# Performance work log

Hardware: AMD Instinct MI355X
Metric: run time of the kernel (lower is better)

Reference implementation:

```python
import jax, jax.numpy as jnp
import numpy as np

B, C, N, H = 4, 256, 2048, 8
D = C // 4  # q/k projection dim
BN_EPS = 1e-5


def setup_inputs() -> dict:
    key = jax.random.key(0)
    ks = jax.random.split(key, 16)
    s = lambda fan: 1.0 / np.sqrt(fan)
    return {
        "x": jax.random.normal(ks[0], (B, C, N), dtype=jnp.float32),
        # per-head params, stacked on leading head axis
        "w_qk": jax.random.normal(ks[1], (H, D, C), dtype=jnp.float32) * s(C),  # shared q/k conv weight
        "w_v": jax.random.normal(ks[2], (H, C, C), dtype=jnp.float32) * s(C),
        "b_v": jax.random.normal(ks[3], (H, C), dtype=jnp.float32) * 0.01,
        "w_t": jax.random.normal(ks[4], (H, C, C), dtype=jnp.float32) * s(C),
        "b_t": jax.random.normal(ks[5], (H, C), dtype=jnp.float32) * 0.01,
        "bn_g": jnp.ones((H, C), dtype=jnp.float32),
        "bn_b": jnp.zeros((H, C), dtype=jnp.float32),
        "bn_m": jax.random.normal(ks[6], (H, C), dtype=jnp.float32) * 0.1,
        "bn_v": jax.random.uniform(ks[7], (H, C), dtype=jnp.float32, minval=0.5, maxval=1.5),
        # final 1x1 conv + BN (LeakyReLU 0.2)
        "w_lin": jax.random.normal(ks[8], (C, C * H), dtype=jnp.float32) * s(C * H),
        "lbn_g": jnp.ones((C,), dtype=jnp.float32),
        "lbn_b": jnp.zeros((C,), dtype=jnp.float32),
        "lbn_m": jax.random.normal(ks[9], (C,), dtype=jnp.float32) * 0.1,
        "lbn_v": jax.random.uniform(ks[10], (C,), dtype=jnp.float32, minval=0.5, maxval=1.5),
    }


def _oa_head(x, w_qk, w_v, b_v, w_t, b_t, g, b, m, v):
    # x: [B, C, N]; 1x1 Conv1d == channel matmul
    x_q = jnp.einsum("dc,bcn->bnd", w_qk, x)                 # [B, N, D]
    x_k = jnp.einsum("dc,bcn->bdn", w_qk, x)                 # [B, D, N] (shared weight)
    x_v = jnp.einsum("ec,bcn->ben", w_v, x) + b_v[:, None]   # [B, C, N]
    energy = jnp.einsum("bnd,bdm->bnm", x_q, x_k)            # [B, N, N]
    attn = jax.nn.softmax(energy, axis=-1)
    attn = attn / (1e-9 + attn.sum(axis=1, keepdims=True))   # extra L1 renorm over dim=1
    x_r = jnp.einsum("ben,bnm->bem", x_v, attn)              # [B, C, N]
    y = jnp.einsum("ec,bcn->ben", w_t, x - x_r) + b_t[:, None]
    y = (y - m[:, None]) * (g[:, None] / jnp.sqrt(v[:, None] + BN_EPS)) + b[:, None]
    return x + jax.nn.relu(y)


def reference(x, w_qk, w_v, b_v, w_t, b_t, bn_g, bn_b, bn_m, bn_v,
              w_lin, lbn_g, lbn_b, lbn_m, lbn_v):
    # run all H heads via vmap over stacked params -> [B, H, C, N]
    heads = jax.vmap(_oa_head, in_axes=(None, 0, 0, 0, 0, 0, 0, 0, 0, 0), out_axes=1)(
        x, w_qk, w_v, b_v, w_t, b_t, bn_g, bn_b, bn_m, bn_v)
    cat = heads.reshape(x.shape[0], H * C, x.shape[2])       # torch.cat(dim=1) order
    y = jnp.einsum("ck,bkn->bcn", w_lin, cat)                # 1x1 conv, no bias
    y = (y - lbn_m[:, None]) * (lbn_g[:, None] / jnp.sqrt(lbn_v[:, None] + BN_EPS)) + lbn_b[:, None]
    return jnp.where(y >= 0, y, 0.2 * y)                     # LeakyReLU(0.2)
```

## Files before the change

kernel.cpp:

```cpp
#include <hip/hip_runtime.h>
#include <math.h>

#define B_ 4
#define C_ 256
#define N_ 2048
#define H_ 8
#define D_ 64
#define BH_ 32
#define HC_ 2048
#define BN_EPS 1e-5f
#define SCL 1.2011224087864498f

typedef __attribute__((ext_vector_type(8))) short s8v;
typedef __attribute__((ext_vector_type(4))) short s4v;
typedef __attribute__((ext_vector_type(8))) _Float16 h8v;
typedef __attribute__((ext_vector_type(4))) _Float16 h4v;
typedef __attribute__((ext_vector_type(4))) float f32x4;

#define MFMA __builtin_amdgcn_mfma_f32_16x16x32_bf16
#define MFMAH __builtin_amdgcn_mfma_f32_16x16x32_f16

static __device__ __forceinline__ unsigned short f2b(float f) {
  union { float f; unsigned int i; } v; v.f = f;
  unsigned int r = v.i + 0x7FFFu + ((v.i >> 16) & 1u);
  return (unsigned short)(r >> 16);
}
static __device__ __forceinline__ float fexp2(float x) {
  float r;
  asm("v_exp_f32 %0, %1" : "=v"(r) : "v"(x));
  return r;
}
static __device__ __forceinline__ unsigned cvtpk(float lo, float hi) {
  unsigned r;
  asm("v_cvt_pk_bf16_f32 %0, %1, %2" : "=v"(r) : "v"(lo), "v"(hi));
  return r;
}
static __device__ __forceinline__ void gload16(const void* g, void* l) {
  __builtin_amdgcn_global_load_lds(
      (const __attribute__((address_space(1))) unsigned int*)g,
      (__attribute__((address_space(3))) unsigned int*)l, 16, 0, 0);
}

struct GP {
  const float *x, *w_qk, *w_v, *b_v, *w_t, *b_t, *bn_g, *bn_b, *bn_m, *bn_v;
  const float *w_lin, *lbn_g, *lbn_b, *lbn_m, *lbn_v;
  _Float16 *PT, *xT, *wqk16, *wvh;
  short *HOT, *wtb, *wlinb, *Vb, *xmr;
  float *part, *shb, *nrm, *sh, *out;
};

__global__ __launch_bounds__(256) void prep_k(GP p) {
  int u = blockIdx.x * 256 + threadIdx.x;
  if (u < 131072) {
    int i = u * 4;
    float4 v = *(const float4*)(p.w_t + i);
    s4v o = { (short)f2b(v.x), (short)f2b(v.y), (short)f2b(v.z), (short)f2b(v.w) };
    *(s4v*)(p.wtb + i) = o;
  } else if (u < 262144) {
    int i = (u - 131072) * 4;
    float4 v = *(const float4*)(p.w_lin + i);
    s4v o = { (short)f2b(v.x), (short)f2b(v.y), (short)f2b(v.z), (short)f2b(v.w) };
    *(s4v*)(p.wlinb + i) = o;
  } else if (u < 393216) {
    int i = (u - 262144) * 4;
    float4 v = *(const float4*)(p.w_v + i);
    h4v o = { (_Float16)v.x, (_Float16)v.y, (_Float16)v.z, (_Float16)v.w };
    *(h4v*)(p.wvh + i) = o;
  } else {
    int i = (u - 393216) * 4;
    float4 v = *(const float4*)(p.w_qk + i);
    h4v o = { (_Float16)v.x, (_Float16)v.y, (_Float16)v.z, (_Float16)v.w };
    *(h4v*)(p.wqk16 + i) = o;
  }
}

__global__ __launch_bounds__(256) void xcvt_k(const float* __restrict__ x,
                                              _Float16* __restrict__ xT) {
  const int n0 = blockIdx.x * 64, c0 = blockIdx.y * 64, b = blockIdx.z;
  const float* xb = x + (size_t)b * C_ * N_;
  __shared__ float sm[64][65];
  const int t = threadIdx.x;
#pragma unroll
  for (int i = 0; i < 4; ++i) {
    int idx = i * 256 + t;
    int c = idx >> 4, j = (idx & 15) * 4;
    float4 v = *(const float4*)(xb + (size_t)(c0 + c) * N_ + n0 + j);
    sm[j + 0][c] = v.x; sm[j + 1][c] = v.y; sm[j + 2][c] = v.z; sm[j + 3][c] = v.w;
  }
  __syncthreads();
#pragma unroll
  for (int i = 0; i < 2; ++i) {
    int idx = i * 256 + t;
    int n = idx >> 3, cg = (idx & 7) * 8;
    h8v o;
#pragma unroll
    for (int d = 0; d < 8; ++d) o[d] = (_Float16)sm[n][cg + d];
    *(h8v*)(xT + ((size_t)b * N_ + n0 + n) * C_ + c0 + cg) = o;
  }
}

__global__ __launch_bounds__(256, 2) void p_k(GP p) {
  const int t = threadIdx.x, wv = t >> 6, lane = t & 63;
  const int l15 = lane & 15, l4 = lane >> 4;
  const int n0 = blockIdx.x * 128;
  const int bh = blockIdx.y, b = bh / H_, h = bh % H_;
  const _Float16* Ag = p.wqk16 + h * D_ * C_;
  const _Float16* Bg = p.xT + (size_t)b * N_ * C_;
  __shared__ _Float16 As[64 * 64], Bs[128 * 64];
  __shared__ float Tr[128 * 65];
  f32x4 acc[4][2] = {};
  for (int kc = 0; kc < 256; kc += 64) {
    __syncthreads();
#pragma unroll
    for (int i = 0; i < 2; ++i) {
      int idx = i * 256 + t;
      int row = idx >> 3, offl = (idx & 7) * 16;
      gload16((const char*)(Ag + (size_t)row * C_ + kc) + (offl ^ ((row & 7) << 4)),
              (char*)As + idx * 16);
    }
#pragma unroll
    for (int i = 0; i < 4; ++i) {
      int idx = i * 256 + t;
      int row = idx >> 3, offl = (idx & 7) * 16;
      gload16((const char*)(Bg + (size_t)(n0 + row) * C_ + kc) + (offl ^ ((row & 7) << 4)),
              (char*)Bs + idx * 16);
    }
    __syncthreads();
    h8v ad[4][2], bn[2][2];
#pragma unroll
    for (int d = 0; d < 4; ++d)
#pragma unroll
      for (int ks = 0; ks < 2; ++ks) {
        int row = d * 16 + l15;
        ad[d][ks] = *(const h8v*)((const char*)As + row * 128 + ((ks * 64 + l4 * 16) ^ ((row & 7) << 4)));
      }
#pragma unroll
    for (int nb = 0; nb < 2; ++nb)
#pragma unroll
      for (int ks = 0; ks < 2; ++ks) {
        int row = wv * 32 + nb * 16 + l15;
        bn[nb][ks] = *(const h8v*)((const char*)Bs + row * 128 + ((ks * 64 + l4 * 16) ^ ((row & 7) << 4)));
      }
#pragma unroll
    for (int d = 0; d < 4; ++d)
#pragma unroll
      for (int nb = 0; nb < 2; ++nb) {
        acc[d][nb] = MFMAH(ad[d][0], bn[nb][0], acc[d][nb], 0, 0, 0);
        acc[d][nb] = MFMAH(ad[d][1], bn[nb][1], acc[d][nb], 0, 0, 0);
      }
  }
  __syncthreads();
#pragma unroll
  for (int d = 0; d < 4; ++d)
#pragma unroll
    for (int nb = 0; nb < 2; ++nb)
#pragma unroll
      for (int r = 0; r < 4; ++r) {
        int n_l = wv * 32 + nb * 16 + l15;
        int dd = d * 16 + l4 * 4 + r;
        Tr[n_l * 65 + dd] = acc[d][nb][r];
      }
  __syncthreads();
  _Float16* Pf = p.PT + ((size_t)bh * N_ + n0) * D_;
  float* nz = p.nrm + (size_t)bh * N_;
#pragma unroll
  for (int i = 0; i < 4; ++i) {
    int idx = i * 256 + t;
    int n = idx >> 3, dg = (idx & 7) * 8;
    h8v hv;
    float ssq = 0.f;
#pragma unroll
    for (int j = 0; j < 8; ++j) {
      float v = Tr[n * 65 + dg + j] * SCL;
      ssq = fmaf(v, v, ssq);
      hv[j] = (_Float16)v;
    }
    *(h8v*)(Pf + (size_t)n * D_ + dg) = hv;
    ssq += __shfl_xor(ssq, 1, 64);
    ssq += __shfl_xor(ssq, 2, 64);
    ssq += __shfl_xor(ssq, 4, 64);
    if ((t & 7) == 0) nz[n0 + n] = ssq;
  }
}

__global__ __launch_bounds__(256) void shift_k(const float* __restrict__ nrm,
                                               float* __restrict__ sh) {
  const int z = blockIdx.x, t = threadIdx.x;
  const float* nz = nrm + (size_t)z * N_;
  float loc[8];
  float mx = 0.f;
#pragma unroll
  for (int i = 0; i < 8; ++i) {
    loc[i] = nz[i * 256 + t];
    mx = fmaxf(mx, loc[i]);
  }
  for (int o = 32; o; o >>= 1) mx = fmaxf(mx, __shfl_xor(mx, o, 64));
  __shared__ float sb[4];
  if ((t & 63) == 0) sb[t >> 6] = mx;
  __syncthreads();
  float M = sqrtf(fmaxf(fmaxf(sb[0], sb[1]), fmaxf(sb[2], sb[3])));
#pragma unroll
  for (int i = 0; i < 8; ++i)
    sh[(size_t)z * N_ + i * 256 + t] = sqrtf(loc[i]) * M;
}

__global__ __launch_bounds__(256, 4) void passa_k(GP p) {
  const int t = threadIdx.x, wv = t >> 6, lane = t & 63;
  const int l15 = lane & 15, l4 = lane >> 4;
  const int wr = wv >> 1, wc = wv & 1;
  const int z = blockIdx.x;
  int idx = blockIdx.y;
  int ti = 0;
  while (idx >= 16 - ti) { idx -= 16 - ti; ++ti; }
  const int tj = ti + idx;
  const int r0 = ti * 128, c0 = tj * 128;
  const _Float16* Pz = p.PT + (size_t)z * N_ * D_;
  const float* shz = p.sh + (size_t)z * N_;
  __shared__ short RH[8192], CH[8192];
  __shared__ float rbuf[2][2][64], cbuf[2][2][64];
#pragma unroll
  for (int i = 0; i < 4; ++i) {
    int c2 = i * 256 + t;
    int row = c2 >> 3, offl = (c2 & 7) * 16;
    int so = offl ^ ((row & 7) << 4);
    gload16((const char*)(Pz + (size_t)(r0 + row) * D_) + so, (char*)RH + c2 * 16);
    if (ti != tj)
      gload16((const char*)(Pz + (size_t)(c0 + row) * D_) + so, (char*)CH + c2 * 16);
  }
  __syncthreads();
  const char* BHp = (ti == tj) ? (const char*)RH : (const char*)CH;

  h8v bh4[4][2];
  float shc[4];
#pragma unroll
  for (int nf = 0; nf < 4; ++nf) {
#pragma unroll
    for (int ks = 0; ks < 2; ++ks) {
      int row = wc * 64 + nf * 16 + l15;
      int byte = row * 128 + ((ks * 64 + l4 * 16) ^ ((row & 7) << 4));
      bh4[nf][ks] = *(const h8v*)(BHp + byte);
    }
    shc[nf] = shz[c0 + wc * 64 + nf * 16 + l15];
  }
  float rowp[4][4] = {};
  float colp[4] = {};
#pragma unroll
  for (int mf = 0; mf < 4; ++mf) {
    h8v ah[2];
#pragma unroll
    for (int ks = 0; ks < 2; ++ks) {
      int row = wr * 64 + mf * 16 + l15;
      int byte = row * 128 + ((ks * 64 + l4 * 16) ^ ((row & 7) << 4));
      ah[ks] = *(const h8v*)((const char*)RH + byte);
    }
    f32x4 shr = *(const f32x4*)(shz + r0 + wr * 64 + mf * 16 + l4 * 4);
#pragma unroll
    for (int nf = 0; nf < 4; ++nf) {
      f32x4 s = {};
      s = MFMAH(ah[0], bh4[nf][0], s, 0, 0, 0);
      s = MFMAH(ah[1], bh4[nf][1], s, 0, 0, 0);
      rowp[mf][0] += fexp2(s[0] - shr[0]);
      rowp[mf][1] += fexp2(s[1] - shr[1]);
      rowp[mf][2] += fexp2(s[2] - shr[2]);
      rowp[mf][3] += fexp2(s[3] - shr[3]);
      if (ti != tj)
        colp[nf] += fexp2(s[0] - shc[nf]) + fexp2(s[1] - shc[nf]) +
                    fexp2(s[2] - shc[nf]) + fexp2(s[3] - shc[nf]);
    }
  }
#pragma unroll
  for (int mf = 0; mf < 4; ++mf)
#pragma unroll
    for (int r = 0; r < 4; ++r) {
      float v = rowp[mf][r];
      v += __shfl_xor(v, 1, 64); v += __shfl_xor(v, 2, 64);
      v += __shfl_xor(v, 4, 64); v += __shfl_xor(v, 8, 64);
      rowp[mf][r] = v;
    }
#pragma unroll
  for (int nf = 0; nf < 4; ++nf) {
    float v = colp[nf];
    v += __shfl_xor(v, 16, 64); v += __shfl_xor(v, 32, 64);
    colp[nf] = v;
  }
  if (l15 == 0)
#pragma unroll
    for (int mf = 0; mf < 4; ++mf)
#pragma unroll
      for (int r = 0; r < 4; ++r)
        rbuf[wr][wc][mf * 16 + l4 * 4 + r] = rowp[mf][r];
  if (l4 == 0)
#pragma unroll
    for (int nf = 0; nf < 4; ++nf)
      cbuf[wc][wr][nf * 16 + l15] = colp[nf];
  __syncthreads();
  if (t < 128) {
    float v = rbuf[t >> 6][0][t & 63] + rbuf[t >> 6][1][t & 63];
    p.part[((size_t)z * 16 + tj) * N_ + r0 + t] = v;
  } else if (ti != tj) {
    int u = t - 128;
    float v = cbuf[u >> 6][0][u & 63] + cbuf[u >> 6][1][u & 63];
    p.part[((size_t)z * 16 + ti) * N_ + c0 + u] = v;
  }
}

__global__ __launch_bounds__(256) void shbred_k(const float* __restrict__ part,
                                                const float* __restrict__ sh,
                                                float* __restrict__ shb) {
  int i = blockIdx.x * 256 + threadIdx.x;
  int z = i >> 11, n = i & 2047;
  const float* pz = part + ((size_t)z * 16) * N_ + n;
  float s = 0.f;
#pragma unroll
  for (int j = 0; j < 16; ++j) s += pz[(size_t)j * N_];
  shb[i] = sh[i] + __log2f(s);
}

__global__ __launch_bounds__(256, 2) void passb_k(GP p) {
  const int t = threadIdx.x, wv = t >> 6, lane = t & 63;
  const int l15 = lane & 15, l4 = lane >> 4;
  const int z = blockIdx.x, b = z / H_;
  const int m0 = blockIdx.y * 128;
  const _Float16* Pz = p.PT + (size_t)z * N_ * D_;
  const short* Vz = p.Vb + (size_t)z * C_ * N_;
  const float* shbz = p.shb + (size_t)z * N_;

  __shared__ char smem[57856];
  float* cs_sm = (float*)(smem + 49152);
  float* shs = (float*)(smem + 49664);

  h8v bm[2][2];
#pragma unroll
  for (int mf = 0; mf < 2; ++mf)
#pragma unroll
    for (int ks = 0; ks < 2; ++ks)
      bm[mf][ks] = *(const h8v*)(Pz + (size_t)(m0 + wv * 32 + mf * 16 + l15) * D_ + ks * 32 + l4 * 8);

  s8v va[4][2];

#define STAGE_PN(n0v, bufbyte) do { \
    _Pragma("unroll") \
    for (int i_ = 0; i_ < 2; ++i_) { \
      int sl_ = i_ * 256 + t; \
      int rw_ = sl_ >> 3, of_ = (sl_ & 7) * 16; \
      gload16((const char*)(Pz + (size_t)((n0v) + rw_) * D_) + (of_ ^ ((rw_ & 7) << 4)), \
              smem + (bufbyte) + sl_ * 16); \
    } \
  } while (0)
#define ISSUE_V(n0v) do { \
    _Pragma("unroll") \
    for (int eb = 0; eb < 4; ++eb) { \
      const short* vr_ = Vz + (size_t)(wv * 64 + eb * 16 + l15) * N_ + (n0v) + l4 * 8; \
      va[eb][0] = *(const s8v*)vr_; \
      va[eb][1] = *(const s8v*)(vr_ + 32); \
    } \
  } while (0)

  f32x4 racc[4][8] = {};
  float csa0 = 0.f, csa1 = 0.f;

  STAGE_PN(0, 0);
  STAGE_PN(64, 8192);
  ISSUE_V(0);
#pragma unroll
  for (int i = 0; i < 2; ++i) {
    int ii = i * 256 + t;
    *(float4*)(shs + ii * 4) = *(const float4*)(shbz + ii * 4);
  }
  __syncthreads();

  for (int it = 0; it < 32; ++it) {
    const int n0 = it * 64;
    const int cur = it & 1;
    const char* PH = smem + cur * 8192;
    char* AT = smem + 16384 + cur * 16384;
#pragma unroll
    for (int nb = 0; nb < 4; ++nb) {
      int rowb = nb * 16 + l15;
      int sw = (rowb & 7) << 4;
      h8v an0 = *(const h8v*)(PH + rowb * 128 + ((l4 * 16) ^ sw));
      h8v an1 = *(const h8v*)(PH + rowb * 128 + ((64 + l4 * 16) ^ sw));
      f32x4 s0 = {}, s1 = {};
      s0 = MFMAH(an0, bm[0][0], s0, 0, 0, 0);
      s0 = MFMAH(an1, bm[0][1], s0, 0, 0, 0);
      s1 = MFMAH(an0, bm[1][0], s1, 0, 0, 0);
      s1 = MFMAH(an1, bm[1][1], s1, 0, 0, 0);
      f32x4 sb4 = *(const f32x4*)(shs + n0 + nb * 16 + l4 * 4);
      float a0 = fexp2(s0[0] - sb4[0]);
      float a1 = fexp2(s0[1] - sb4[1]);
      float a2 = fexp2(s0[2] - sb4[2]);
      float a3 = fexp2(s0[3] - sb4[3]);
      float c0 = fexp2(s1[0] - sb4[0]);
      float c1 = fexp2(s1[1] - sb4[1]);
      float c2 = fexp2(s1[2] - sb4[2]);
      float c3 = fexp2(s1[3] - sb4[3]);
      csa0 += (a0 + a1) + (a2 + a3);
      csa1 += (c0 + c1) + (c2 + c3);
      uint2 pk0 = { cvtpk(a0, a1), cvtpk(a2, a3) };
      uint2 pk1 = { cvtpk(c0, c1), cvtpk(c2, c3) };
      int swm = (l15 & 7) << 4;
      int cb = (nb * 32 + l4 * 8);
      *(uint2*)(AT + (wv * 32 + l15) * 128 + (cb ^ swm)) = pk0;
      *(uint2*)(AT + (wv * 32 + 16 + l15) * 128 + (cb ^ swm)) = pk1;
    }
    asm volatile("s_waitcnt vmcnt(8) lgkmcnt(0)" ::: "memory");
    __builtin_amdgcn_s_barrier();
    __builtin_amdgcn_sched_barrier(0);
    if (it < 30) STAGE_PN(n0 + 128, cur * 8192);
    __builtin_amdgcn_s_setprio(1);
#pragma unroll
    for (int mb = 0; mb < 8; ++mb) {
      int rowb = mb * 16 + l15;
      int sw = (rowb & 7) << 4;
      s8v at0 = *(const s8v*)(AT + rowb * 128 + ((l4 * 16) ^ sw));
      s8v at1 = *(const s8v*)(AT + rowb * 128 + ((64 + l4 * 16) ^ sw));
#pragma unroll
      for (int eb = 0; eb < 4; ++eb) {
        racc[eb][mb] = MFMA(va[eb][0], at0, racc[eb][mb], 0, 0, 0);
        racc[eb][mb] = MFMA(va[eb][1], at1, racc[eb][mb], 0, 0, 0);
      }
    }
    __builtin_amdgcn_s_setprio(0);
    if (it < 31) ISSUE_V(n0 + 64);
  }

  csa0 += __shfl_xor(csa0, 16, 64);
  csa0 += __shfl_xor(csa0, 32, 64);
  csa1 += __shfl_xor(csa1, 16, 64);
  csa1 += __shfl_xor(csa1, 32, 64);
  if (l4 == 0) {
    cs_sm[wv * 32 + l15] = csa0;
    cs_sm[wv * 32 + 16 + l15] = csa1;
  }
  __syncthreads();
  float invc[8];
#pragma unroll
  for (int mb = 0; mb < 8; ++mb) invc[mb] = 1.0f / (1e-9f + cs_sm[mb * 16 + l15]);
  const float* xb = p.x + (size_t)b * C_ * N_;
  char* Tr = smem;
#pragma unroll
  for (int half = 0; half < 2; ++half) {
    if (half) __syncthreads();
#pragma unroll
    for (int eb = 0; eb < 4; ++eb)
#pragma unroll
      for (int mbh = 0; mbh < 4; ++mbh) {
        int mb = half * 4 + mbh;
        int e0 = wv * 64 + eb * 16 + l4 * 4;
        int m_l = mbh * 16 + l15;
        int mg = m0 + mb * 16 + l15;
        float v0 = xb[(size_t)(e0 + 0) * N_ + mg] - racc[eb][mb][0] * invc[mb];
        float v1 = xb[(size_t)(e0 + 1) * N_ + mg] - racc[eb][mb][1] * invc[mb];
        float v2 = xb[(size_t)(e0 + 2) * N_ + mg] - racc[eb][mb][2] * invc[mb];
        float v3 = xb[(size_t)(e0 + 3) * N_ + mg] - racc[eb][mb][3] * invc[mb];
        uint2 pk = { cvtpk(v0, v1), cvtpk(v2, v3) };
        *(uint2*)(Tr + m_l * 512 + ((e0 * 2) ^ ((m_l & 7) << 4))) = pk;
      }
    __syncthreads();
    short* xz = p.xmr + ((size_t)z * N_ + m0 + half * 64) * C_;
#pragma unroll
    for (int i = 0; i < 8; ++i) {
      int idx = i * 256 + t;
      int m_l = idx >> 5, off2 = (idx & 31) * 16;
      s8v v = *(const s8v*)(Tr + m_l * 512 + (off2 ^ ((m_l & 7) << 4)));
      *(s8v*)((char*)(xz + (size_t)m_l * C_) + off2) = v;
    }
  }
#undef STAGE_PN
#undef ISSUE_V
}

template<int EPI>
__global__ __launch_bounds__(256) void mm_k(GP p) {
  constexpr int K = 256;
  const int t = threadIdx.x;
  const int wave = t >> 6, lane = t & 63;
  const int wr = wave >> 1, wc = wave & 1;
  const int l15 = lane & 15, l4 = lane >> 4;
  const int n0 = blockIdx.x * 128;
  const int m0 = blockIdx.y * 128;
  const int z = blockIdx.z;
  int b = z / H_, h = z % H_;

  const short *Ag, *Bg;
  if constexpr (EPI == 1) {
    Ag = (const short*)(p.wvh + (size_t)h * C_ * C_);
    Bg = (const short*)(p.xT + (size_t)b * N_ * C_);
  } else {
    Ag = p.wtb + (size_t)h * C_ * C_;
    Bg = p.xmr + (size_t)z * N_ * C_;
  }

  __shared__ short As[2][128 * 32];
  __shared__ short Bs[2][128 * 32];

  f32x4 acc[4][4] = {};

#define STAGE_MM(ksv, bufv) do { \
    int k0_ = (ksv) * 32; \
    _Pragma("unroll") \
    for (int i_ = 0; i_ < 2; ++i_) { \
      int idx_ = i_ * 256 + t; \
      int row_ = idx_ >> 2, kg_ = (idx_ & 3) * 8; \
      gload16(Ag + (size_t)(m0 + row_) * K + k0_ + kg_, (char*)As[bufv] + idx_ * 16); \
      gload16(Bg + (size_t)(n0 + row_) * K + k0_ + kg_, (char*)Bs[bufv] + idx_ * 16); \
    } \
  } while (0)

  STAGE_MM(0, 0);
  asm volatile("s_waitcnt vmcnt(0)" ::: "memory");
  __builtin_amdgcn_s_barrier();
  __builtin_amdgcn_sched_barrier(0);

  for (int ks = 0; ks < 8; ++ks) {
    const int cur = ks & 1;
    if (ks < 7) STAGE_MM(ks + 1, cur ^ 1);
    s8v af[4], bf[4];
#pragma unroll
    for (int m = 0; m < 4; ++m) af[m] = *(const s8v*)&As[cur][(wr * 64 + m * 16 + l15) * 32 + l4 * 8];
#pragma unroll
    for (int n = 0; n < 4; ++n) bf[n] = *(const s8v*)&Bs[cur][(wc * 64 + n * 16 + l15) * 32 + l4 * 8];
#pragma unroll
    for (int m = 0; m < 4; ++m)
#pragma unroll
      for (int n = 0; n < 4; ++n) {
        if constexpr (EPI == 1)
          acc[m][n] = MFMAH(__builtin_bit_cast(h8v, af[m]), __builtin_bit_cast(h8v, bf[n]),
                            acc[m][n], 0, 0, 0);
        else
          acc[m][n] = MFMA(af[m], bf[n], acc[m][n], 0, 0, 0);
      }
    asm volatile("s_waitcnt vmcnt(0) lgkmcnt(0)" ::: "memory");
    __builtin_amdgcn_s_barrier();
    __builtin_amdgcn_sched_barrier(0);
  }
#undef STAGE_MM

  if constexpr (EPI == 1) {
    short* Vz = p.Vb + (size_t)z * C_ * N_;
#pragma unroll
    for (int m = 0; m < 4; ++m)
#pragma unroll
      for (int r = 0; r < 4; ++r) {
        int e = m0 + wr * 64 + m * 16 + l4 * 4 + r;
        float bias = p.b_v[h * C_ + e];
#pragma unroll
        for (int n = 0; n < 4; ++n) {
          int c = n0 + wc * 64 + n * 16 + l15;
          Vz[(size_t)e * N_ + c] = (short)f2b(acc[m][n][r] + bias);
        }
      }
  } else {
    __shared__ short Tr[128 * 128];
    const float* xb = p.x + (size_t)b * C_ * N_;
#pragma unroll
    for (int m = 0; m < 4; ++m)
#pragma unroll
      for (int r = 0; r < 4; ++r) {
        int e = m0 + wr * 64 + m * 16 + l4 * 4 + r;
        int el = e - m0;
        int hc = h * C_ + e;
        float bt = p.b_t[hc], mm = p.bn_m[hc], bb = p.bn_b[hc];
        float sc = p.bn_g[hc] / sqrtf(p.bn_v[hc] + BN_EPS);
#pragma unroll
        for (int n = 0; n < 4; ++n) {
          int cl = wc * 64 + n * 16 + l15;
          float y = (acc[m][n][r] + bt - mm) * sc + bb;
          float val = xb[(size_t)e * N_ + n0 + cl] + fmaxf(y, 0.f);
          Tr[cl * 128 + el] = (short)f2b(val);
        }
      }
    __syncthreads();
    short* Hz = p.HOT + (size_t)b * N_ * HC_;
#pragma unroll
    for (int it = 0; it < 8; ++it) {
      int idx = it * 256 + t;
      int cl = idx >> 4, eg = (idx & 15) * 8;
      *(s8v*)(Hz + (size_t)(n0 + cl) * HC_ + h * C_ + m0 + eg) = *(const s8v*)&Tr[cl * 128 + eg];
    }
  }
}

__global__ __launch_bounds__(256) void mm4_k(GP p) {
  const int t = threadIdx.x, wv = t >> 6, lane = t & 63;
  const int l15 = lane & 15, l4 = lane >> 4;
  const int n0 = blockIdx.x * 128;
  const int m0 = blockIdx.y * 64;
  const int b = blockIdx.z;
  const short* Ag = p.wlinb;
  const short* Bg = p.HOT + (size_t)b * N_ * HC_;
  __shared__ short As[2][64 * 64], Bs[2][128 * 64];
  f32x4 acc[4][2] = {};

#define STAGE_M4(k0v, bufv) do { \
    _Pragma("unroll") \
    for (int i_ = 0; i_ < 2; ++i_) { \
      int sl_ = i_ * 256 + t; \
      int rw_ = sl_ >> 3, of_ = (sl_ & 7) * 16; \
      gload16((const char*)(Ag + (size_t)(m0 + rw_) * HC_ + (k0v)) + (of_ ^ ((rw_ & 7) << 4)), \
              (char*)As[bufv] + sl_ * 16); \
    } \
    _Pragma("unroll") \
    for (int i_ = 0; i_ < 4; ++i_) { \
      int sl_ = i_ * 256 + t; \
      int rw_ = sl_ >> 3, of_ = (sl_ & 7) * 16; \
      gload16((const char*)(Bg + (size_t)(n0 + rw_) * HC_ + (k0v)) + (of_ ^ ((rw_ & 7) << 4)), \
              (char*)Bs[bufv] + sl_ * 16); \
    } \
  } while (0)

  STAGE_M4(0, 0);
  asm volatile("s_waitcnt vmcnt(0)" ::: "memory");
  __builtin_amdgcn_s_barrier();
  __builtin_amdgcn_sched_barrier(0);

  for (int ks = 0; ks < 32; ++ks) {
    const int cur = ks & 1;
    if (ks < 31) STAGE_M4((ks + 1) * 64, cur ^ 1);
    s8v af[4][2], bf[2][2];
#pragma unroll
    for (int m = 0; m < 4; ++m)
#pragma unroll
      for (int k2 = 0; k2 < 2; ++k2) {
        int rw = m * 16 + l15;
        af[m][k2] = *(const s8v*)((const char*)As[cur] + rw * 128 + ((k2 * 64 + l4 * 16) ^ ((rw & 7) << 4)));
      }
#pragma unroll
    for (int nf = 0; nf < 2; ++nf)
#pragma unroll
      for (int k2 = 0; k2 < 2; ++k2) {
        int rw = wv * 32 + nf * 16 + l15;
        bf[nf][k2] = *(const s8v*)((const char*)Bs[cur] + rw * 128 + ((k2 * 64 + l4 * 16) ^ ((rw & 7) << 4)));
      }
#pragma unroll
    for (int m = 0; m < 4; ++m)
#pragma unroll
      for (int nf = 0; nf < 2; ++nf) {
        acc[m][nf] = MFMA(af[m][0], bf[nf][0], acc[m][nf], 0, 0, 0);
        acc[m][nf] = MFMA(af[m][1], bf[nf][1], acc[m][nf], 0, 0, 0);
      }
    asm volatile("s_waitcnt vmcnt(0) lgkmcnt(0)" ::: "memory");
    __builtin_amdgcn_s_barrier();
    __builtin_amdgcn_sched_barrier(0);
  }
#undef STAGE_M4

  float* ob = p.out + (size_t)b * C_ * N_;
#pragma unroll
  for (int m = 0; m < 4; ++m)
#pragma unroll
    for (int r = 0; r < 4; ++r) {
      int e = m0 + m * 16 + l4 * 4 + r;
      float mm = p.lbn_m[e], bb = p.lbn_b[e];
      float sc = p.lbn_g[e] / sqrtf(p.lbn_v[e] + BN_EPS);
#pragma unroll
      for (int nf = 0; nf < 2; ++nf) {
        int c = n0 + wv * 32 + nf * 16 + l15;
        float y = (acc[m][nf][r] - mm) * sc + bb;
        ob[(size_t)e * N_ + c] = y >= 0.f ? y : 0.2f * y;
      }
    }
}

extern "C" void kernel_launch(void* const* d_in, const int* in_sizes, int n_in,
                              void* d_out, int out_size, void* d_ws, size_t ws_size,
                              hipStream_t stream) {
  GP p;
  p.x     = (const float*)d_in[0];
  p.w_qk  = (const float*)d_in[1];
  p.w_v   = (const float*)d_in[2];
  p.b_v   = (const float*)d_in[3];
  p.w_t   = (const float*)d_in[4];
  p.b_t   = (const float*)d_in[5];
  p.bn_g  = (const float*)d_in[6];
  p.bn_b  = (const float*)d_in[7];
  p.bn_m  = (const float*)d_in[8];
  p.bn_v  = (const float*)d_in[9];
  p.w_lin = (const float*)d_in[10];
  p.lbn_g = (const float*)d_in[11];
  p.lbn_b = (const float*)d_in[12];
  p.lbn_m = (const float*)d_in[13];
  p.lbn_v = (const float*)d_in[14];
  p.out   = (float*)d_out;

  char* base = (char*)d_ws;
  size_t off = 0;
  auto alloc = [&](size_t bytes) -> char* {
    char* r = base + off;
    off += (bytes + 255) & ~(size_t)255;
    return r;
  };
  p.PT    = (_Float16*)alloc((size_t)BH_ * N_ * D_ * 2);
  p.xT    = (_Float16*)alloc((size_t)B_ * N_ * C_ * 2);
  p.wqk16 = (_Float16*)alloc((size_t)H_ * D_ * C_ * 2);
  p.wvh   = (_Float16*)alloc((size_t)H_ * C_ * C_ * 2);
  p.wtb   = (short*)alloc((size_t)H_ * C_ * C_ * 2);
  p.wlinb = (short*)alloc((size_t)C_ * HC_ * 2);
  p.Vb    = (short*)alloc((size_t)BH_ * C_ * N_ * 2);
  p.xmr   = (short*)alloc((size_t)BH_ * N_ * C_ * 2);
  p.part  = (float*)alloc((size_t)BH_ * 16 * N_ * 4);
  p.shb   = (float*)alloc((size_t)BH_ * N_ * 4);
  p.nrm   = (float*)alloc((size_t)BH_ * N_ * 4);
  p.sh    = (float*)alloc((size_t)BH_ * N_ * 4);
  p.HOT   = p.Vb;

  dim3 blk(256);

  prep_k<<<1664, blk, 0, stream>>>(p);
  xcvt_k<<<dim3(32, 4, B_), blk, 0, stream>>>(p.x, p.xT);
  p_k<<<dim3(16, BH_), blk, 0, stream>>>(p);
  shift_k<<<BH_, blk, 0, stream>>>(p.nrm, p.sh);
  mm_k<1><<<dim3(16, 2, BH_), blk, 0, stream>>>(p);
  passa_k<<<dim3(32, 136), blk, 0, stream>>>(p);
  shbred_k<<<256, blk, 0, stream>>>(p.part, p.sh, p.shb);
  passb_k<<<dim3(32, 16), blk, 0, stream>>>(p);
  mm_k<3><<<dim3(16, 2, BH_), blk, 0, stream>>>(p);
  mm4_k<<<dim3(16, 4, B_), blk, 0, stream>>>(p);
}
```

Baseline: 232.2 us.

## Halve passb output tile to 64 columns for more blocks and occupancy

Each passb block now handles 64 output columns instead of 128. That halves the accumulator registers and LDS per block, doubles the grid to 32x32 blocks, and raises the launch bound to 3 blocks per CU. The aim is better occupancy and more blocks across the GPU's compute units. In exchange, each block re-streams the full V and P tiles for half as much output, which doubles global and LDS traffic for those operands and halves MFMA work per loaded V fragment.

```diff
diff --git a/kernel.cpp b/kernel.cpp
--- a/kernel.cpp
+++ b/kernel.cpp
@@ -316,25 +316,23 @@
   shb[i] = sh[i] + __log2f(s);
 }
 
-__global__ __launch_bounds__(256, 2) void passb_k(GP p) {
+__global__ __launch_bounds__(256, 3) void passb_k(GP p) {
   const int t = threadIdx.x, wv = t >> 6, lane = t & 63;
   const int l15 = lane & 15, l4 = lane >> 4;
   const int z = blockIdx.x, b = z / H_;
-  const int m0 = blockIdx.y * 128;
+  const int m0 = blockIdx.y * 64;
   const _Float16* Pz = p.PT + (size_t)z * N_ * D_;
   const short* Vz = p.Vb + (size_t)z * C_ * N_;
   const float* shbz = p.shb + (size_t)z * N_;
 
-  __shared__ char smem[57856];
-  float* cs_sm = (float*)(smem + 49152);
-  float* shs = (float*)(smem + 49664);
-
-  h8v bm[2][2];
-#pragma unroll
-  for (int mf = 0; mf < 2; ++mf)
-#pragma unroll
-    for (int ks = 0; ks < 2; ++ks)
-      bm[mf][ks] = *(const h8v*)(Pz + (size_t)(m0 + wv * 32 + mf * 16 + l15) * D_ + ks * 32 + l4 * 8);
+  __shared__ char smem[41472];
+  float* cs_sm = (float*)(smem + 32768);
+  float* shs = (float*)(smem + 33024);
+
+  h8v bm[2];
+#pragma unroll
+  for (int ks = 0; ks < 2; ++ks)
+    bm[ks] = *(const h8v*)(Pz + (size_t)(m0 + wv * 16 + l15) * D_ + ks * 32 + l4 * 8);
 
   s8v va[4][2];
 
@@ -356,8 +354,8 @@
     } \
   } while (0)
 
-  f32x4 racc[4][8] = {};
-  float csa0 = 0.f, csa1 = 0.f;
+  f32x4 racc[4][4] = {};
+  float csacc = 0.f;
 
   STAGE_PN(0, 0);
   STAGE_PN(64, 8192);
@@ -369,39 +367,29 @@
   }
   __syncthreads();
 
+  const int mrow = wv * 16 + l15;
   for (int it = 0; it < 32; ++it) {
     const int n0 = it * 64;
     const int cur = it & 1;
     const char* PH = smem + cur * 8192;
-    char* AT = smem + 16384 + cur * 16384;
+    char* AT = smem + 16384 + cur * 8192;
 #pragma unroll
     for (int nb = 0; nb < 4; ++nb) {
       int rowb = nb * 16 + l15;
       int sw = (rowb & 7) << 4;
       h8v an0 = *(const h8v*)(PH + rowb * 128 + ((l4 * 16) ^ sw));
       h8v an1 = *(const h8v*)(PH + rowb * 128 + ((64 + l4 * 16) ^ sw));
-      f32x4 s0 = {}, s1 = {};
-      s0 = MFMAH(an0, bm[0][0], s0, 0, 0, 0);
-      s0 = MFMAH(an1, bm[0][1], s0, 0, 0, 0);
-      s1 = MFMAH(an0, bm[1][0], s1, 0, 0, 0);
-      s1 = MFMAH(an1, bm[1][1], s1, 0, 0, 0);
+      f32x4 s0 = {};
+      s0 = MFMAH(an0, bm[0], s0, 0, 0, 0);
+      s0 = MFMAH(an1, bm[1], s0, 0, 0, 0);
       f32x4 sb4 = *(const f32x4*)(shs + n0 + nb * 16 + l4 * 4);
       float a0 = fexp2(s0[0] - sb4[0]);
       float a1 = fexp2(s0[1] - sb4[1]);
       float a2 = fexp2(s0[2] - sb4[2]);
       float a3 = fexp2(s0[3] - sb4[3]);
-      float c0 = fexp2(s1[0] - sb4[0]);
-      float c1 = fexp2(s1[1] - sb4[1]);
-      float c2 = fexp2(s1[2] - sb4[2]);
-      float c3 = fexp2(s1[3] - sb4[3]);
-      csa0 += (a0 + a1) + (a2 + a3);
-      csa1 += (c0 + c1) + (c2 + c3);
+      csacc += (a0 + a1) + (a2 + a3);
       uint2 pk0 = { cvtpk(a0, a1), cvtpk(a2, a3) };
-      uint2 pk1 = { cvtpk(c0, c1), cvtpk(c2, c3) };
-      int swm = (l15 & 7) << 4;
-      int cb = (nb * 32 + l4 * 8);
-      *(uint2*)(AT + (wv * 32 + l15) * 128 + (cb ^ swm)) = pk0;
-      *(uint2*)(AT + (wv * 32 + 16 + l15) * 128 + (cb ^ swm)) = pk1;
+      *(uint2*)(AT + mrow * 128 + ((nb * 32 + l4 * 8) ^ ((mrow & 7) << 4))) = pk0;
     }
     asm volatile("s_waitcnt vmcnt(8) lgkmcnt(0)" ::: "memory");
     __builtin_amdgcn_s_barrier();
@@ -409,7 +397,7 @@
     if (it < 30) STAGE_PN(n0 + 128, cur * 8192);
     __builtin_amdgcn_s_setprio(1);
 #pragma unroll
-    for (int mb = 0; mb < 8; ++mb) {
+    for (int mb = 0; mb < 4; ++mb) {
       int rowb = mb * 16 + l15;
       int sw = (rowb & 7) << 4;
       s8v at0 = *(const s8v*)(AT + rowb * 128 + ((l4 * 16) ^ sw));
@@ -424,47 +412,37 @@
     if (it < 31) ISSUE_V(n0 + 64);
   }
 
-  csa0 += __shfl_xor(csa0, 16, 64);
-  csa0 += __shfl_xor(csa0, 32, 64);
-  csa1 += __shfl_xor(csa1, 16, 64);
-  csa1 += __shfl_xor(csa1, 32, 64);
-  if (l4 == 0) {
-    cs_sm[wv * 32 + l15] = csa0;
-    cs_sm[wv * 32 + 16 + l15] = csa1;
-  }
-  __syncthreads();
-  float invc[8];
-#pragma unroll
-  for (int mb = 0; mb < 8; ++mb) invc[mb] = 1.0f / (1e-9f + cs_sm[mb * 16 + l15]);
+  csacc += __shfl_xor(csacc, 16, 64);
+  csacc += __shfl_xor(csacc, 32, 64);
+  if (l4 == 0) cs_sm[mrow] = csacc;
+  __syncthreads();
+  float invc[4];
+#pragma unroll
+  for (int mb = 0; mb < 4; ++mb) invc[mb] = 1.0f / (1e-9f + cs_sm[mb * 16 + l15]);
   const float* xb = p.x + (size_t)b * C_ * N_;
   char* Tr = smem;
 #pragma unroll
-  for (int half = 0; half < 2; ++half) {
-    if (half) __syncthreads();
-#pragma unroll
-    for (int eb = 0; eb < 4; ++eb)
-#pragma unroll
-      for (int mbh = 0; mbh < 4; ++mbh) {
-        int mb = half * 4 + mbh;
-        int e0 = wv * 64 + eb * 16 + l4 * 4;
-        int m_l = mbh * 16 + l15;
-        int mg = m0 + mb * 16 + l15;
-        float v0 = xb[(size_t)(e0 + 0) * N_ + mg] - racc[eb][mb][0] * invc[mb];
-        float v1 = xb[(size_t)(e0 + 1) * N_ + mg] - racc[eb][mb][1] * invc[mb];
-        float v2 = xb[(size_t)(e0 + 2) * N_ + mg] - racc[eb][mb][2] * invc[mb];
-        float v3 = xb[(size_t)(e0 + 3) * N_ + mg] - racc[eb][mb][3] * invc[mb];
-        uint2 pk = { cvtpk(v0, v1), cvtpk(v2, v3) };
-        *(uint2*)(Tr + m_l * 512 + ((e0 * 2) ^ ((m_l & 7) << 4))) = pk;
-      }
-    __syncthreads();
-    short* xz = p.xmr + ((size_t)z * N_ + m0 + half * 64) * C_;
-#pragma unroll
-    for (int i = 0; i < 8; ++i) {
-      int idx = i * 256 + t;
-      int m_l = idx >> 5, off2 = (idx & 31) * 16;
-      s8v v = *(const s8v*)(Tr + m_l * 512 + (off2 ^ ((m_l & 7) << 4)));
-      *(s8v*)((char*)(xz + (size_t)m_l * C_) + off2) = v;
-    }
+  for (int eb = 0; eb < 4; ++eb)
+#pragma unroll
+    for (int mb = 0; mb < 4; ++mb) {
+      int e0 = wv * 64 + eb * 16 + l4 * 4;
+      int m_l = mb * 16 + l15;
+      int mg = m0 + m_l;
+      float v0 = xb[(size_t)(e0 + 0) * N_ + mg] - racc[eb][mb][0] * invc[mb];
+      float v1 = xb[(size_t)(e0 + 1) * N_ + mg] - racc[eb][mb][1] * invc[mb];
+      float v2 = xb[(size_t)(e0 + 2) * N_ + mg] - racc[eb][mb][2] * invc[mb];
+      float v3 = xb[(size_t)(e0 + 3) * N_ + mg] - racc[eb][mb][3] * invc[mb];
+      uint2 pk = { cvtpk(v0, v1), cvtpk(v2, v3) };
+      *(uint2*)(Tr + m_l * 512 + ((e0 * 2) ^ ((m_l & 7) << 4))) = pk;
+    }
+  __syncthreads();
+  short* xz = p.xmr + ((size_t)z * N_ + m0) * C_;
+#pragma unroll
+  for (int i = 0; i < 8; ++i) {
+    int idx = i * 256 + t;
+    int m_l = idx >> 5, off2 = (idx & 31) * 16;
+    s8v v = *(const s8v*)(Tr + m_l * 512 + (off2 ^ ((m_l & 7) << 4)));
+    *(s8v*)((char*)(xz + (size_t)m_l * C_) + off2) = v;
   }
 #undef STAGE_PN
 #undef ISSUE_V
@@ -713,7 +691,7 @@
   mm_k<1><<<dim3(16, 2, BH_), blk, 0, stream>>>(p);
   passa_k<<<dim3(32, 136), blk, 0, stream>>>(p);
   shbred_k<<<256, blk, 0, stream>>>(p.part, p.sh, p.shb);
-  passb_k<<<dim3(32, 16), blk, 0, stream>>>(p);
+  passb_k<<<dim3(32, 32), blk, 0, stream>>>(p);
   mm_k<3><<<dim3(16, 2, BH_), blk, 0, stream>>>(p);
   mm4_k<<<dim3(16, 4, B_), blk, 0, stream>>>(p);
 }
```

Result: slower. 299.3 us (+28.9%).
